# Performance work log

Hardware: AMD Instinct MI355X
Metric: run time of the kernel (lower is better)

The kernel has to match this reference:

```python
import jax, jax.numpy as jnp
import numpy as np

C, H, P = 128, 4, 8  # d_model, n_heads, n_points (n_levels=1)
D = C // H


def setup_inputs() -> dict:
    key = jax.random.key(0)
    ks = jax.random.split(key, 14)
    B, Y, X = 2, 200, 200
    N = Y * X
    s = 0.05
    inp = {
        "query": jax.random.normal(ks[0], (B, N, C), jnp.float32),
        "query_pos": jax.random.normal(ks[1], (B, N, C), jnp.float32),
        # MSDeformAttn params
        "Wv": jax.random.normal(ks[2], (C, C), jnp.float32) * s,
        "bv": jnp.zeros((C,), jnp.float32),
        "Woff": jax.random.normal(ks[3], (C, H * P * 2), jnp.float32) * s,
        "boff": jax.random.normal(ks[4], (H * P * 2,), jnp.float32) * s,
        "Wattn": jax.random.normal(ks[5], (C, H * P), jnp.float32) * s,
        "battn": jnp.zeros((H * P,), jnp.float32),
        "Wout1": jax.random.normal(ks[6], (C, C), jnp.float32) * s,  # MSDeformAttn.output_proj
        "bout1": jnp.zeros((C,), jnp.float32),
        "Wout2": jax.random.normal(ks[7], (C, C), jnp.float32) * s,  # wrapper output_proj
        "bout2": jnp.zeros((C,), jnp.float32),
        "Y": Y,
        "X": X,
    }
    return inp


def _deform_attn(q, v_in, Wv, bv, Woff, boff, Wattn, battn, Wout1, bout1, Y, X):
    B, N, _ = q.shape
    # reference points: grid centers, stacked (y, x) normalized (as in source)
    ref_y = (jnp.arange(Y, dtype=jnp.float32) + 0.5) / Y
    ref_x = (jnp.arange(X, dtype=jnp.float32) + 0.5) / X
    ry, rx = jnp.meshgrid(ref_y, ref_x, indexing="ij")
    ref = jnp.stack([ry.reshape(-1), rx.reshape(-1)], -1)  # (N, 2)

    value = (v_in @ Wv + bv).reshape(B, Y, X, H, D).transpose(0, 3, 1, 2, 4)  # (B,H,Y,X,D)
    off = (q @ Woff + boff).reshape(B, N, H, P, 2)
    attn = jax.nn.softmax((q @ Wattn + battn).reshape(B, N, H, P), axis=-1)

    # offset normalizer = (W, H) = (X, Y); loc = ref + off/norm  (faithful to source)
    norm = jnp.array([X, Y], jnp.float32)
    loc = ref[None, :, None, None, :] + off / norm  # (B,N,H,P,2)

    # grid_sample bilinear, align_corners=False, zero padding; channel 0 = x, 1 = y
    gx = loc[..., 0] * X - 0.5
    gy = loc[..., 1] * Y - 0.5
    x0 = jnp.floor(gx)
    y0 = jnp.floor(gy)
    wx1 = gx - x0
    wy1 = gy - y0
    x0i = x0.astype(jnp.int32)
    y0i = y0.astype(jnp.int32)

    b_idx = jnp.arange(B)[:, None, None, None]
    h_idx = jnp.arange(H)[None, None, :, None]

    def gather(yi, xi, w):
        valid = (yi >= 0) & (yi < Y) & (xi >= 0) & (xi < X)
        yc = jnp.clip(yi, 0, Y - 1)
        xc = jnp.clip(xi, 0, X - 1)
        v = value[b_idx, h_idx, yc, xc]  # (B,N,H,P,D)
        return v * (w * valid)[..., None]

    sampled = (
        gather(y0i, x0i, (1 - wy1) * (1 - wx1))
        + gather(y0i, x0i + 1, (1 - wy1) * wx1)
        + gather(y0i + 1, x0i, wy1 * (1 - wx1))
        + gather(y0i + 1, x0i + 1, wy1 * wx1)
    )
    out = (sampled * attn[..., None]).sum(axis=3).reshape(B, N, C)
    return out @ Wout1 + bout1


def reference(query, query_pos, Wv, bv, Woff, boff, Wattn, battn, Wout1, bout1, Wout2, bout2, Y, X):
    residual = query
    q = query + query_pos
    out = _deform_attn(q, q, Wv, bv, Woff, boff, Wattn, battn, Wout1, bout1, Y, X)
    out = out @ Wout2 + bout2  # wrapper output_proj; dropout in eval mode = identity
    return out + residual
```

## Files before the change

### kernel.cpp

```cpp
#include <hip/hip_runtime.h>
#include <hip/hip_bf16.h>
#include <hip/hip_fp16.h>

#define BQ 2
#define YY 200
#define XX 200
#define NQ 40000
#define CC 128
#define MTOT 80000
#define NCOL 224
#define NTILES 5000

typedef __attribute__((ext_vector_type(8))) short short8;
typedef __attribute__((ext_vector_type(4))) short short4v;
typedef __attribute__((ext_vector_type(4))) float f32x4;

static __device__ __forceinline__ unsigned short f2bf(float f) {
    union { float f; unsigned int u; } v; v.f = f;
    unsigned int r = v.u + 0x7FFF + ((v.u >> 16) & 1);
    return (unsigned short)(r >> 16);
}
static __device__ __forceinline__ unsigned short f2bf_hw(float f) {
    __hip_bfloat16 h = __float2bfloat16(f);
    unsigned short s;
    __builtin_memcpy(&s, &h, 2);
    return s;
}
static __device__ __forceinline__ __half2 u2h2(unsigned int u) {
    __half2 h; __builtin_memcpy(&h, &u, 4); return h;
}
static __device__ __forceinline__ unsigned int h22u(__half2 h) {
    unsigned int u; __builtin_memcpy(&u, &h, 4); return u;
}
static __device__ __forceinline__ short h2s(__half h) {
    short s; __builtin_memcpy(&s, &h, 2); return s;
}
static __device__ __forceinline__ unsigned int packh2(float a, float b) {
    return h22u(__floats2half2_rn(a, b));
}

__global__ void prep_wcat(const float* __restrict__ Wv, const float* __restrict__ Woff,
                          const float* __restrict__ Wattn, unsigned short* __restrict__ WcatT) {
    int idx = blockIdx.x * 256 + threadIdx.x;
    if (idx >= NCOL * CC) return;
    int c = idx >> 7, k = idx & 127;
    float w = (c < 128) ? Wv[k * 128 + c]
            : (c < 192) ? Woff[k * 64 + (c - 128)]
                        : Wattn[k * 32 + (c - 192)];
    WcatT[c * 128 + k] = f2bf(w);
}

__global__ void prep_w12(const float* __restrict__ Wout1, const float* __restrict__ Wout2,
                         const float* __restrict__ bout1, const float* __restrict__ bout2,
                         unsigned short* __restrict__ W12T, float* __restrict__ b12) {
    int idx = blockIdx.x * 256 + threadIdx.x;
    int c = idx >> 7, k = idx & 127;
    float s = 0.f;
    for (int j = 0; j < 128; ++j) s += Wout1[k * 128 + j] * Wout2[j * 128 + c];
    W12T[c * 128 + k] = f2bf(s);
    if (k == 0) {
        float t = bout2[c];
        for (int j = 0; j < 128; ++j) t += bout1[j] * Wout2[j * 128 + c];
        b12[c] = t;
    }
}

__global__ __launch_bounds__(256) void qsum_kernel(const float* __restrict__ query,
                                                   const float* __restrict__ qpos,
                                                   unsigned short* __restrict__ qbf) {
    const size_t total = (size_t)MTOT * CC / 8;
    for (size_t c = (size_t)blockIdx.x * 256 + threadIdx.x; c < total;
         c += (size_t)gridDim.x * 256) {
        const float4* a = (const float4*)(query + c * 8);
        const float4* b = (const float4*)(qpos + c * 8);
        float4 a0 = a[0], a1 = a[1], b0 = b[0], b1 = b[1];
        short8 w;
        w[0] = (short)f2bf_hw(a0.x + b0.x); w[1] = (short)f2bf_hw(a0.y + b0.y);
        w[2] = (short)f2bf_hw(a0.z + b0.z); w[3] = (short)f2bf_hw(a0.w + b0.w);
        w[4] = (short)f2bf_hw(a1.x + b1.x); w[5] = (short)f2bf_hw(a1.y + b1.y);
        w[6] = (short)f2bf_hw(a1.z + b1.z); w[7] = (short)f2bf_hw(a1.w + b1.w);
        *(short8*)(qbf + c * 8) = w;
    }
}

__global__ __launch_bounds__(256, 2) void g1_kernel(
    const unsigned short* __restrict__ qbf, const unsigned short* __restrict__ WcatT,
    const float* __restrict__ bv, const float* __restrict__ boff, const float* __restrict__ battn,
    unsigned short* __restrict__ value_h, unsigned short* __restrict__ off_h,
    unsigned short* __restrict__ logits_h)
{
    const int tid = threadIdx.x;
    const int group = blockIdx.x >> 8;
    const int gblk = blockIdx.x & 255;
    const int lane = tid & 63;
    const int arow = lane & 15, kq = lane >> 4;
    const int wid = gblk * 4 + (tid >> 6);
    const int tg0 = group * 4;
    const int NT = (group == 3) ? 2 : 4;

    short8 bf[4][4];
#pragma unroll
    for (int t = 0; t < 4; ++t) {
        if (t < NT) {
#pragma unroll
            for (int ks = 0; ks < 4; ++ks)
                bf[t][ks] = *(const short8*)(WcatT + (size_t)((tg0 + t) * 16 + arow) * 128 + ks * 32 + kq * 8);
        }
    }

    f32x4 biasv[4];
#pragma unroll
    for (int t = 0; t < 4; ++t) {
        if (t < NT) {
            const float* bp = (group < 2) ? (bv + (tg0 + t) * 16 + kq * 4)
                            : (group == 2) ? (boff + (tg0 + t - 8) * 16 + kq * 4)
                                           : (battn + (tg0 + t - 12) * 16 + kq * 4);
            float4 b4 = *(const float4*)bp;
            biasv[t] = (f32x4){b4.x, b4.y, b4.z, b4.w};
        }
    }

    for (int tile = wid; tile < NTILES; tile += 1024) {
        const char* pa = (const char*)qbf + (size_t)(tile * 16 + arow) * 256 + kq * 16;
        short8 af[4];
#pragma unroll
        for (int ks = 0; ks < 4; ++ks) af[ks] = *(const short8*)(pa + ks * 64);

        f32x4 acc[4];
#pragma unroll
        for (int t = 0; t < 4; ++t) acc[t] = biasv[t];

#pragma unroll
        for (int ks = 0; ks < 4; ++ks) {
#pragma unroll
            for (int t = 0; t < 4; ++t) {
                if (t < NT)
                    acc[t] = __builtin_amdgcn_mfma_f32_16x16x32_bf16(bf[t][ks], af[ks], acc[t], 0, 0, 0);
            }
        }

        const int row = tile * 16 + arow;
        if (group < 2) {
#pragma unroll
            for (int t = 0; t < 4; ++t) {
                short4v pv;
                pv[0] = h2s(__float2half(acc[t][0])); pv[1] = h2s(__float2half(acc[t][1]));
                pv[2] = h2s(__float2half(acc[t][2])); pv[3] = h2s(__float2half(acc[t][3]));
                *(short4v*)(value_h + (size_t)row * 128 + (tg0 + t) * 16 + kq * 4) = pv;
            }
        } else if (group == 2) {
#pragma unroll
            for (int t = 0; t < 4; ++t) {
                uint2 pk;
                pk.x = packh2(acc[t][0], acc[t][1]);
                pk.y = packh2(acc[t][2], acc[t][3]);
                *(uint2*)(off_h + (size_t)row * 64 + (tg0 + t - 8) * 16 + kq * 4) = pk;
            }
        } else {
#pragma unroll
            for (int t = 0; t < 2; ++t) {
                uint2 pk;
                pk.x = packh2(acc[t][0], acc[t][1]);
                pk.y = packh2(acc[t][2], acc[t][3]);
                *(uint2*)(logits_h + (size_t)row * 32 + (tg0 + t - 12) * 16 + kq * 4) = pk;
            }
        }
    }
}

__global__ __launch_bounds__(256) void sample_kernel(
    const unsigned short* __restrict__ value_h, const unsigned short* __restrict__ off_h,
    const unsigned short* __restrict__ logits_h, unsigned short* __restrict__ sampled)
{
    __shared__ int4 SA[8][36];
    __shared__ int4 SW[8][36];

    const int tid = threadIdx.x;
    const int qi = tid >> 5;
    const int lane = tid & 31;
    const int r = blockIdx.x * 8 + qi;
    const int b = (r >= NQ) ? 1 : 0;
    const int n = r - b * NQ;
    const int yq = n / XX, xq = n - yq * XX;

    {
        float lg = __half2float(*(const __half*)(logits_h + (size_t)r * 32 + lane));
        float m = lg;
        m = fmaxf(m, __shfl_xor(m, 1));
        m = fmaxf(m, __shfl_xor(m, 2));
        m = fmaxf(m, __shfl_xor(m, 4));
        float e = __expf(lg - m);
        float s = e;
        s += __shfl_xor(s, 1);
        s += __shfl_xor(s, 2);
        s += __shfl_xor(s, 4);
        float aw = e / s;

        __half2 oh = u2h2(*(const unsigned int*)(off_h + (size_t)r * 64 + lane * 2));
        float gx = (float)yq + __low2float(oh);
        float gy = (float)xq + __high2float(oh);
        float fx = floorf(gx), fy = floorf(gy);
        int x0 = (int)fx, y0 = (int)fy;
        float wx1 = gx - fx, wy1 = gy - fy;
        float vx0 = ((unsigned)x0 < XX) ? 1.f : 0.f;
        float vx1 = ((unsigned)(x0 + 1) < XX) ? 1.f : 0.f;
        float vy0 = ((unsigned)y0 < YY) ? 1.f : 0.f;
        float vy1 = ((unsigned)(y0 + 1) < YY) ? 1.f : 0.f;
        int x0c = min(max(x0, 0), XX - 1);
        int x1c = min(max(x0 + 1, 0), XX - 1);
        int y0c = min(max(y0, 0), YY - 1);
        int y1c = min(max(y0 + 1, 0), YY - 1);
        int hb = (lane >> 3) * 64;
        int rowA = y0c * XX, rowB = y1c * XX;
        int4 addrs;
        addrs.x = (rowA + x0c) * 256 + hb;
        addrs.y = (rowA + x1c) * 256 + hb;
        addrs.z = (rowB + x0c) * 256 + hb;
        addrs.w = (rowB + x1c) * 256 + hb;

        float wxa = (1.f - wx1) * vx0;
        float wxb = wx1 * vx1;
        float wya = aw * (1.f - wy1) * vy0;
        float wyb = aw * wy1 * vy1;
        int4 wts;
        wts.x = (int)h22u(__float2half2_rn(wxa * wya));
        wts.y = (int)h22u(__float2half2_rn(wxb * wya));
        wts.z = (int)h22u(__float2half2_rn(wxa * wyb));
        wts.w = (int)h22u(__float2half2_rn(wxb * wyb));

        const int slot = (lane & 7) * 4 + (lane >> 3);
        SA[qi][slot] = addrs;
        SW[qi][slot] = wts;
    }
    __syncthreads();

    const char* vb = (const char*)(value_h + (size_t)b * NQ * 128);
    const int h = lane >> 3, yc = (lane >> 2) & 1, quad = lane & 3;
    const int cb = quad * 16;

    int2 a[8];
#pragma unroll
    for (int p = 0; p < 8; ++p)
        a[p] = *(const int2*)((const char*)&SA[qi][p * 4 + h] + yc * 8);

    uint4 d0[8], d1[8];
#pragma unroll
    for (int p = 0; p < 8; ++p) {
        d0[p] = *(const uint4*)(vb + a[p].x + cb);
        d1[p] = *(const uint4*)(vb + a[p].y + cb);
    }

    int2 w[8];
#pragma unroll
    for (int p = 0; p < 8; ++p)
        w[p] = *(const int2*)((const char*)&SW[qi][p * 4 + h] + yc * 8);

    __half2 acc0 = __float2half2_rn(0.f), acc1 = __float2half2_rn(0.f);
    __half2 acc2 = __float2half2_rn(0.f), acc3 = __float2half2_rn(0.f);

#pragma unroll
    for (int p = 0; p < 8; ++p) {
        __half2 wa = u2h2((unsigned int)w[p].x);
        __half2 wb = u2h2((unsigned int)w[p].y);
        acc0 = __hfma2(wa, u2h2(d0[p].x), acc0);
        acc1 = __hfma2(wa, u2h2(d0[p].y), acc1);
        acc2 = __hfma2(wa, u2h2(d0[p].z), acc2);
        acc3 = __hfma2(wa, u2h2(d0[p].w), acc3);
        acc0 = __hfma2(wb, u2h2(d1[p].x), acc0);
        acc1 = __hfma2(wb, u2h2(d1[p].y), acc1);
        acc2 = __hfma2(wb, u2h2(d1[p].z), acc2);
        acc3 = __hfma2(wb, u2h2(d1[p].w), acc3);
    }

    acc0 = __hadd2(acc0, u2h2((unsigned int)__shfl_xor((int)h22u(acc0), 4)));
    acc1 = __hadd2(acc1, u2h2((unsigned int)__shfl_xor((int)h22u(acc1), 4)));
    acc2 = __hadd2(acc2, u2h2((unsigned int)__shfl_xor((int)h22u(acc2), 4)));
    acc3 = __hadd2(acc3, u2h2((unsigned int)__shfl_xor((int)h22u(acc3), 4)));

    __half2 pa = (yc == 0) ? acc0 : acc2;
    __half2 pb = (yc == 0) ? acc1 : acc3;
    uint2 packed;
    packed.x = ((unsigned int)f2bf(__high2float(pa)) << 16) | (unsigned int)f2bf(__low2float(pa));
    packed.y = ((unsigned int)f2bf(__high2float(pb)) << 16) | (unsigned int)f2bf(__low2float(pb));
    *(uint2*)((char*)(sampled + (size_t)r * 128) + h * 64 + cb + yc * 8) = packed;
}

__global__ __launch_bounds__(256, 2) void g2_kernel(
    const unsigned short* __restrict__ sampled, const unsigned short* __restrict__ W12T,
    const float* __restrict__ b12, const float* __restrict__ query, float* __restrict__ out)
{
    const int tid = threadIdx.x;
    const int group = blockIdx.x >> 9;
    const int gblk = blockIdx.x & 511;
    const int lane = tid & 63;
    const int arow = lane & 15, kq = lane >> 4;
    const int wid = gblk * 4 + (tid >> 6);
    const int tg0 = group * 4;

    short8 bf[4][4];
#pragma unroll
    for (int t = 0; t < 4; ++t)
#pragma unroll
        for (int ks = 0; ks < 4; ++ks)
            bf[t][ks] = *(const short8*)(W12T + (size_t)((tg0 + t) * 16 + arow) * 128 + ks * 32 + kq * 8);

    f32x4 biasv[4];
#pragma unroll
    for (int t = 0; t < 4; ++t) {
        float4 b4 = *(const float4*)(b12 + (tg0 + t) * 16 + kq * 4);
        biasv[t] = (f32x4){b4.x, b4.y, b4.z, b4.w};
    }

    for (int tile = wid; tile < NTILES; tile += 2048) {
        const char* pa = (const char*)sampled + (size_t)(tile * 16 + arow) * 256 + kq * 16;
        short8 af[4];
#pragma unroll
        for (int ks = 0; ks < 4; ++ks) af[ks] = *(const short8*)(pa + ks * 64);

        f32x4 acc[4];
#pragma unroll
        for (int t = 0; t < 4; ++t) acc[t] = biasv[t];

#pragma unroll
        for (int ks = 0; ks < 4; ++ks)
#pragma unroll
            for (int t = 0; t < 4; ++t)
                acc[t] = __builtin_amdgcn_mfma_f32_16x16x32_bf16(bf[t][ks], af[ks], acc[t], 0, 0, 0);

        const int row = tile * 16 + arow;
#pragma unroll
        for (int t = 0; t < 4; ++t) {
            size_t idx = (size_t)row * 128 + (tg0 + t) * 16 + kq * 4;
            float4 q4 = *(const float4*)(query + idx);
            float4 o = make_float4(acc[t][0] + q4.x, acc[t][1] + q4.y,
                                   acc[t][2] + q4.z, acc[t][3] + q4.w);
            *(float4*)(out + idx) = o;
        }
    }
}

extern "C" void kernel_launch(void* const* d_in, const int* in_sizes, int n_in,
                              void* d_out, int out_size, void* d_ws, size_t ws_size,
                              hipStream_t stream) {
    const float* query = (const float*)d_in[0];
    const float* qpos  = (const float*)d_in[1];
    const float* Wv    = (const float*)d_in[2];
    const float* bv    = (const float*)d_in[3];
    const float* Woff  = (const float*)d_in[4];
    const float* boff  = (const float*)d_in[5];
    const float* Wattn = (const float*)d_in[6];
    const float* battn = (const float*)d_in[7];
    const float* Wout1 = (const float*)d_in[8];
    const float* bout1 = (const float*)d_in[9];
    const float* Wout2 = (const float*)d_in[10];
    const float* bout2 = (const float*)d_in[11];
    float* out = (float*)d_out;

    char* ws = (char*)d_ws;
    unsigned short* value_h  = (unsigned short*)(ws);
    unsigned short* off_h    = (unsigned short*)(ws + 20480000);
    unsigned short* logits_h = (unsigned short*)(ws + 40960000);
    unsigned short* sampled  = (unsigned short*)(ws + 51200000);
    unsigned short* WcatT    = (unsigned short*)(ws + 71680000);
    unsigned short* W12T     = (unsigned short*)(ws + 71680000 + 57344);
    float*          b12      = (float*)(ws + 71680000 + 57344 + 32768);

    unsigned short* qbf = sampled;

    prep_wcat<<<112, 256, 0, stream>>>(Wv, Woff, Wattn, WcatT);
    prep_w12<<<64, 256, 0, stream>>>(Wout1, Wout2, bout1, bout2, W12T, b12);
    qsum_kernel<<<2048, 256, 0, stream>>>(query, qpos, qbf);
    g1_kernel<<<1024, 256, 0, stream>>>(qbf, WcatT, bv, boff, battn,
                                        value_h, off_h, logits_h);
    sample_kernel<<<MTOT / 8, 256, 0, stream>>>(value_h, off_h, logits_h, sampled);
    g2_kernel<<<1024, 256, 0, stream>>>(sampled, W12T, b12, query, out);
}
```

Baseline: 109.8 us.

## Fuse bilinear sampling with output projection GEMM via LDS tile

Merges the sampling kernel and the final projection GEMM into one kernel. Each block now handles 16 queries and writes the sampled bf16 rows to an LDS tile, then 8 waves each compute one 16-column MFMA slice and add the residual. This removes the global write and re-read of the sampled buffer and one launch. The two weight-prep kernels are also merged into a single launch. In exchange, every block reloads its W12 fragments, and each wave does only four MFMAs after a block-wide barrier.

```diff
diff --git a/kernel.cpp b/kernel.cpp
--- a/kernel.cpp
+++ b/kernel.cpp
@@ -39,29 +39,31 @@
     return h22u(__floats2half2_rn(a, b));
 }
 
-__global__ void prep_wcat(const float* __restrict__ Wv, const float* __restrict__ Woff,
-                          const float* __restrict__ Wattn, unsigned short* __restrict__ WcatT) {
-    int idx = blockIdx.x * 256 + threadIdx.x;
-    if (idx >= NCOL * CC) return;
-    int c = idx >> 7, k = idx & 127;
-    float w = (c < 128) ? Wv[k * 128 + c]
-            : (c < 192) ? Woff[k * 64 + (c - 128)]
-                        : Wattn[k * 32 + (c - 192)];
-    WcatT[c * 128 + k] = f2bf(w);
-}
-
-__global__ void prep_w12(const float* __restrict__ Wout1, const float* __restrict__ Wout2,
-                         const float* __restrict__ bout1, const float* __restrict__ bout2,
-                         unsigned short* __restrict__ W12T, float* __restrict__ b12) {
-    int idx = blockIdx.x * 256 + threadIdx.x;
-    int c = idx >> 7, k = idx & 127;
-    float s = 0.f;
-    for (int j = 0; j < 128; ++j) s += Wout1[k * 128 + j] * Wout2[j * 128 + c];
-    W12T[c * 128 + k] = f2bf(s);
-    if (k == 0) {
-        float t = bout2[c];
-        for (int j = 0; j < 128; ++j) t += bout1[j] * Wout2[j * 128 + c];
-        b12[c] = t;
+__global__ void prep_kernel(const float* __restrict__ Wv, const float* __restrict__ Woff,
+                            const float* __restrict__ Wattn,
+                            const float* __restrict__ Wout1, const float* __restrict__ Wout2,
+                            const float* __restrict__ bout1, const float* __restrict__ bout2,
+                            unsigned short* __restrict__ WcatT,
+                            unsigned short* __restrict__ W12T, float* __restrict__ b12) {
+    if (blockIdx.x < 112) {
+        int idx = blockIdx.x * 256 + threadIdx.x;
+        if (idx >= NCOL * CC) return;
+        int c = idx >> 7, k = idx & 127;
+        float w = (c < 128) ? Wv[k * 128 + c]
+                : (c < 192) ? Woff[k * 64 + (c - 128)]
+                            : Wattn[k * 32 + (c - 192)];
+        WcatT[c * 128 + k] = f2bf(w);
+    } else {
+        int idx = (blockIdx.x - 112) * 256 + threadIdx.x;
+        int c = idx >> 7, k = idx & 127;
+        float s = 0.f;
+        for (int j = 0; j < 128; ++j) s += Wout1[k * 128 + j] * Wout2[j * 128 + c];
+        W12T[c * 128 + k] = f2bf(s);
+        if (k == 0) {
+            float t = bout2[c];
+            for (int j = 0; j < 128; ++j) t += bout1[j] * Wout2[j * 128 + c];
+            b12[c] = t;
+        }
     }
 }
 
@@ -168,17 +170,19 @@
     }
 }
 
-__global__ __launch_bounds__(256) void sample_kernel(
+__global__ __launch_bounds__(512, 2) void sg2_kernel(
     const unsigned short* __restrict__ value_h, const unsigned short* __restrict__ off_h,
-    const unsigned short* __restrict__ logits_h, unsigned short* __restrict__ sampled)
+    const unsigned short* __restrict__ logits_h, const unsigned short* __restrict__ W12T,
+    const float* __restrict__ b12, const float* __restrict__ query, float* __restrict__ out)
 {
-    __shared__ int4 SA[8][36];
-    __shared__ int4 SW[8][36];
+    __shared__ int4 SA[16][36];
+    __shared__ int4 SW[16][36];
+    __shared__ unsigned char Stile[16 * 272];
 
     const int tid = threadIdx.x;
     const int qi = tid >> 5;
     const int lane = tid & 31;
-    const int r = blockIdx.x * 8 + qi;
+    const int r = blockIdx.x * 16 + qi;
     const int b = (r >= NQ) ? 1 : 0;
     const int n = r - b * NQ;
     const int yq = n / XX, xq = n - yq * XX;
@@ -234,108 +238,86 @@
     }
     __syncthreads();
 
-    const char* vb = (const char*)(value_h + (size_t)b * NQ * 128);
-    const int h = lane >> 3, yc = (lane >> 2) & 1, quad = lane & 3;
-    const int cb = quad * 16;
-
-    int2 a[8];
-#pragma unroll
-    for (int p = 0; p < 8; ++p)
-        a[p] = *(const int2*)((const char*)&SA[qi][p * 4 + h] + yc * 8);
-
-    uint4 d0[8], d1[8];
-#pragma unroll
-    for (int p = 0; p < 8; ++p) {
-        d0[p] = *(const uint4*)(vb + a[p].x + cb);
-        d1[p] = *(const uint4*)(vb + a[p].y + cb);
-    }
-
-    int2 w[8];
-#pragma unroll
-    for (int p = 0; p < 8; ++p)
-        w[p] = *(const int2*)((const char*)&SW[qi][p * 4 + h] + yc * 8);
-
-    __half2 acc0 = __float2half2_rn(0.f), acc1 = __float2half2_rn(0.f);
-    __half2 acc2 = __float2half2_rn(0.f), acc3 = __float2half2_rn(0.f);
-
-#pragma unroll
-    for (int p = 0; p < 8; ++p) {
-        __half2 wa = u2h2((unsigned int)w[p].x);
-        __half2 wb = u2h2((unsigned int)w[p].y);
-        acc0 = __hfma2(wa, u2h2(d0[p].x), acc0);
-        acc1 = __hfma2(wa, u2h2(d0[p].y), acc1);
-        acc2 = __hfma2(wa, u2h2(d0[p].z), acc2);
-        acc3 = __hfma2(wa, u2h2(d0[p].w), acc3);
-        acc0 = __hfma2(wb, u2h2(d1[p].x), acc0);
-        acc1 = __hfma2(wb, u2h2(d1[p].y), acc1);
-        acc2 = __hfma2(wb, u2h2(d1[p].z), acc2);
-        acc3 = __hfma2(wb, u2h2(d1[p].w), acc3);
-    }
-
-    acc0 = __hadd2(acc0, u2h2((unsigned int)__shfl_xor((int)h22u(acc0), 4)));
-    acc1 = __hadd2(acc1, u2h2((unsigned int)__shfl_xor((int)h22u(acc1), 4)));
-    acc2 = __hadd2(acc2, u2h2((unsigned int)__shfl_xor((int)h22u(acc2), 4)));
-    acc3 = __hadd2(acc3, u2h2((unsigned int)__shfl_xor((int)h22u(acc3), 4)));
-
-    __half2 pa = (yc == 0) ? acc0 : acc2;
-    __half2 pb = (yc == 0) ? acc1 : acc3;
-    uint2 packed;
-    packed.x = ((unsigned int)f2bf(__high2float(pa)) << 16) | (unsigned int)f2bf(__low2float(pa));
-    packed.y = ((unsigned int)f2bf(__high2float(pb)) << 16) | (unsigned int)f2bf(__low2float(pb));
-    *(uint2*)((char*)(sampled + (size_t)r * 128) + h * 64 + cb + yc * 8) = packed;
-}
-
-__global__ __launch_bounds__(256, 2) void g2_kernel(
-    const unsigned short* __restrict__ sampled, const unsigned short* __restrict__ W12T,
-    const float* __restrict__ b12, const float* __restrict__ query, float* __restrict__ out)
-{
-    const int tid = threadIdx.x;
-    const int group = blockIdx.x >> 9;
-    const int gblk = blockIdx.x & 511;
-    const int lane = tid & 63;
-    const int arow = lane & 15, kq = lane >> 4;
-    const int wid = gblk * 4 + (tid >> 6);
-    const int tg0 = group * 4;
-
-    short8 bf[4][4];
-#pragma unroll
-    for (int t = 0; t < 4; ++t)
+    {
+        const char* vb = (const char*)(value_h + (size_t)b * NQ * 128);
+        const int h = lane >> 3, yc = (lane >> 2) & 1, quad = lane & 3;
+        const int cb = quad * 16;
+
+        int2 a[8];
+#pragma unroll
+        for (int p = 0; p < 8; ++p)
+            a[p] = *(const int2*)((const char*)&SA[qi][p * 4 + h] + yc * 8);
+
+        uint4 d0[8], d1[8];
+#pragma unroll
+        for (int p = 0; p < 8; ++p) {
+            d0[p] = *(const uint4*)(vb + a[p].x + cb);
+            d1[p] = *(const uint4*)(vb + a[p].y + cb);
+        }
+
+        int2 w[8];
+#pragma unroll
+        for (int p = 0; p < 8; ++p)
+            w[p] = *(const int2*)((const char*)&SW[qi][p * 4 + h] + yc * 8);
+
+        __half2 acc0 = __float2half2_rn(0.f), acc1 = __float2half2_rn(0.f);
+        __half2 acc2 = __float2half2_rn(0.f), acc3 = __float2half2_rn(0.f);
+
+#pragma unroll
+        for (int p = 0; p < 8; ++p) {
+            __half2 wa = u2h2((unsigned int)w[p].x);
+            __half2 wb = u2h2((unsigned int)w[p].y);
+            acc0 = __hfma2(wa, u2h2(d0[p].x), acc0);
+            acc1 = __hfma2(wa, u2h2(d0[p].y), acc1);
+            acc2 = __hfma2(wa, u2h2(d0[p].z), acc2);
+            acc3 = __hfma2(wa, u2h2(d0[p].w), acc3);
+            acc0 = __hfma2(wb, u2h2(d1[p].x), acc0);
+            acc1 = __hfma2(wb, u2h2(d1[p].y), acc1);
+            acc2 = __hfma2(wb, u2h2(d1[p].z), acc2);
+            acc3 = __hfma2(wb, u2h2(d1[p].w), acc3);
+        }
+
+        acc0 = __hadd2(acc0, u2h2((unsigned int)__shfl_xor((int)h22u(acc0), 4)));
+        acc1 = __hadd2(acc1, u2h2((unsigned int)__shfl_xor((int)h22u(acc1), 4)));
+        acc2 = __hadd2(acc2, u2h2((unsigned int)__shfl_xor((int)h22u(acc2), 4)));
+        acc3 = __hadd2(acc3, u2h2((unsigned int)__shfl_xor((int)h22u(acc3), 4)));
+
+        __half2 pa = (yc == 0) ? acc0 : acc2;
+        __half2 pb = (yc == 0) ? acc1 : acc3;
+        uint2 packed;
+        packed.x = ((unsigned int)f2bf(__high2float(pa)) << 16) | (unsigned int)f2bf(__low2float(pa));
+        packed.y = ((unsigned int)f2bf(__high2float(pb)) << 16) | (unsigned int)f2bf(__low2float(pb));
+        *(uint2*)(Stile + qi * 272 + h * 64 + cb + yc * 8) = packed;
+    }
+    __syncthreads();
+
+    {
+        const int w = tid >> 6;
+        const int lane64 = tid & 63;
+        const int arow = lane64 & 15, kq = lane64 >> 4;
+        const int qbase = blockIdx.x * 16;
+
+        short8 bfr[4];
 #pragma unroll
         for (int ks = 0; ks < 4; ++ks)
-            bf[t][ks] = *(const short8*)(W12T + (size_t)((tg0 + t) * 16 + arow) * 128 + ks * 32 + kq * 8);
-
-    f32x4 biasv[4];
-#pragma unroll
-    for (int t = 0; t < 4; ++t) {
-        float4 b4 = *(const float4*)(b12 + (tg0 + t) * 16 + kq * 4);
-        biasv[t] = (f32x4){b4.x, b4.y, b4.z, b4.w};
-    }
-
-    for (int tile = wid; tile < NTILES; tile += 2048) {
-        const char* pa = (const char*)sampled + (size_t)(tile * 16 + arow) * 256 + kq * 16;
+            bfr[ks] = *(const short8*)(W12T + (size_t)(w * 16 + arow) * 128 + ks * 32 + kq * 8);
+
+        float4 b4 = *(const float4*)(b12 + w * 16 + kq * 4);
+        f32x4 acc = (f32x4){b4.x, b4.y, b4.z, b4.w};
+
         short8 af[4];
 #pragma unroll
-        for (int ks = 0; ks < 4; ++ks) af[ks] = *(const short8*)(pa + ks * 64);
-
-        f32x4 acc[4];
-#pragma unroll
-        for (int t = 0; t < 4; ++t) acc[t] = biasv[t];
-
-#pragma unroll
         for (int ks = 0; ks < 4; ++ks)
-#pragma unroll
-            for (int t = 0; t < 4; ++t)
-                acc[t] = __builtin_amdgcn_mfma_f32_16x16x32_bf16(bf[t][ks], af[ks], acc[t], 0, 0, 0);
-
-        const int row = tile * 16 + arow;
-#pragma unroll
-        for (int t = 0; t < 4; ++t) {
-            size_t idx = (size_t)row * 128 + (tg0 + t) * 16 + kq * 4;
-            float4 q4 = *(const float4*)(query + idx);
-            float4 o = make_float4(acc[t][0] + q4.x, acc[t][1] + q4.y,
-                                   acc[t][2] + q4.z, acc[t][3] + q4.w);
-            *(float4*)(out + idx) = o;
-        }
+            af[ks] = *(const short8*)(Stile + arow * 272 + ks * 64 + kq * 16);
+
+#pragma unroll
+        for (int ks = 0; ks < 4; ++ks)
+            acc = __builtin_amdgcn_mfma_f32_16x16x32_bf16(bfr[ks], af[ks], acc, 0, 0, 0);
+
+        size_t idx = (size_t)(qbase + arow) * 128 + w * 16 + kq * 4;
+        float4 q4 = *(const float4*)(query + idx);
+        float4 o = make_float4(acc[0] + q4.x, acc[1] + q4.y, acc[2] + q4.z, acc[3] + q4.w);
+        *(float4*)(out + idx) = o;
     }
 }
 
@@ -360,18 +342,15 @@
     unsigned short* value_h  = (unsigned short*)(ws);
     unsigned short* off_h    = (unsigned short*)(ws + 20480000);
     unsigned short* logits_h = (unsigned short*)(ws + 40960000);
-    unsigned short* sampled  = (unsigned short*)(ws + 51200000);
+    unsigned short* qbf      = (unsigned short*)(ws + 51200000);
     unsigned short* WcatT    = (unsigned short*)(ws + 71680000);
     unsigned short* W12T     = (unsigned short*)(ws + 71680000 + 57344);
     float*          b12      = (float*)(ws + 71680000 + 57344 + 32768);
 
-    unsigned short* qbf = sampled;
-
-    prep_wcat<<<112, 256, 0, stream>>>(Wv, Woff, Wattn, WcatT);
-    prep_w12<<<64, 256, 0, stream>>>(Wout1, Wout2, bout1, bout2, W12T, b12);
+    prep_kernel<<<176, 256, 0, stream>>>(Wv, Woff, Wattn, Wout1, Wout2, bout1, bout2,
+                                         WcatT, W12T, b12);
     qsum_kernel<<<2048, 256, 0, stream>>>(query, qpos, qbf);
     g1_kernel<<<1024, 256, 0, stream>>>(qbf, WcatT, bv, boff, battn,
                                         value_h, off_h, logits_h);
-    sample_kernel<<<MTOT / 8, 256, 0, stream>>>(value_h, off_h, logits_h, sampled);
-    g2_kernel<<<1024, 256, 0, stream>>>(sampled, W12T, b12, query, out);
-}
+    sg2_kernel<<<NTILES, 512, 0, stream>>>(value_h, off_h, logits_h, W12T, b12, query, out);
+}
```

Result: faster. 104.5 us (-4.8%).
